# Performance work log

Measured on AMD Instinct MI355X. Metric: run time of the kernel, lower is better.

The kernel has to match this reference:

```python
import jax, jax.numpy as jnp
import numpy as np

B, C, W, H = 4, 256, 64, 64
N = W * H
SCALE = 0.02  # keep QK^T energies in a stable softmax range


def setup_inputs() -> dict:
    key = jax.random.key(0)
    ks = jax.random.split(key, 8)
    return {
        "x": jax.random.normal(ks[0], (B, C, W, H), jnp.float32),
        "geo_embed": jax.random.normal(ks[1], (B, N, C), jnp.float32),
        "Wq": jax.random.normal(ks[2], (C, C), jnp.float32) * SCALE,
        "bq": jnp.zeros((C,), jnp.float32),
        "Wk": jax.random.normal(ks[3], (C, C), jnp.float32) * SCALE,
        "bk": jnp.zeros((C,), jnp.float32),
        "Wv": jax.random.normal(ks[4], (C, C), jnp.float32) * SCALE,
        "bv": jnp.zeros((C,), jnp.float32),
        "Wgp": jax.random.normal(ks[5], (C, C), jnp.float32) * SCALE,
        "bgp": jnp.zeros((C,), jnp.float32),
        "Wgg": jax.random.normal(ks[6], (1, 2 * C), jnp.float32) * SCALE,
        "bgg": jnp.zeros((1,), jnp.float32),
    }


def reference(x, geo_embed, Wq, bq, Wk, bk, Wv, bv, Wgp, bgp, Wgg, bgg):
    b, c, w, h = x.shape
    n = w * h
    xf = x.reshape(b, c, n)  # [B, C, N]

    # 1x1 conv == per-pixel linear; q laid out [B, N, O] (permuted in torch)
    q = jnp.einsum("oc,bcn->bno", Wq, xf) + bq  # [B, N, O]

    # geo gating on the query
    ge = geo_embed @ Wgp.T + bgp  # [B, N, O]
    gate = jax.nn.sigmoid(jnp.concatenate([q, ge], axis=-1) @ Wgg.T + bgg)  # [B, N, 1]
    q = q + gate * ge

    k = jnp.einsum("oc,bcn->bon", Wk, xf) + bk[:, None]  # [B, O, N]
    v = jnp.einsum("oc,bcn->bon", Wv, xf) + bv[:, None]  # [B, C, N]

    energy = jnp.einsum("bno,bom->bnm", q, k)  # [B, N, N]
    attention = jax.nn.softmax(energy, axis=-1)

    # out = bmm(value, attention^T): out[b,c,m] = sum_n v[b,c,n] * attention[b,m,n]
    out = jnp.einsum("bcn,bmn->bcm", v, attention).reshape(b, c, w, h)

    # output gating: torch .view reinterpretation of (B, N, O) as (B, C, W, H)
    ge_r = ge.reshape(b, c, w, h)
    out = out * (1.0 + jax.nn.sigmoid(ge_r))
    return out, attention
```

## Files before the change

### kernel.cpp

```cpp
#include <hip/hip_runtime.h>
#include <hip/hip_bf16.h>
#include <math.h>

static constexpr int BB = 4;
static constexpr int CC = 256;
static constexpr int NN = 4096;

using bf16   = __bf16;
using f16    = _Float16;
using bf16x8 = __attribute__((ext_vector_type(8))) __bf16;
using bf16x4 = __attribute__((ext_vector_type(4))) __bf16;
using f16x8  = __attribute__((ext_vector_type(8))) _Float16;
using f16x4  = __attribute__((ext_vector_type(4))) _Float16;
using f32x4  = __attribute__((ext_vector_type(4))) float;

__device__ inline void gload_lds16(const void* g, void* l) {
  __builtin_amdgcn_global_load_lds(
      (const __attribute__((address_space(1))) void*)g,
      (__attribute__((address_space(3))) void*)l, 16, 0, 0);
}

__device__ inline void swz_bid(int& xb, int& yb, int& zb) {
  int gx = gridDim.x, gy = gridDim.y;
  int nwg = gx * gy * (int)gridDim.z;
  int flat = blockIdx.x + gx * (blockIdx.y + gy * blockIdx.z);
  int q = nwg >> 3;
  int w = (flat & 7) * q + (flat >> 3);
  xb = w % gx;
  int r = w / gx;
  yb = r % gy;
  zb = r / gy;
}

__global__ __launch_bounds__(256) void cvt_weights_kernel(
    const float* __restrict__ w0, const float* __restrict__ w1,
    const float* __restrict__ w2, const float* __restrict__ w3,
    bf16* __restrict__ out) {
  const float* srcs[4] = {w0, w1, w2, w3};
  const float* s = srcs[blockIdx.y];
  bf16* dst = out + (size_t)blockIdx.y * (CC * CC);
  int i = (blockIdx.x * 256 + threadIdx.x) * 4;
  float4 v = *(const float4*)(s + i);
  bf16x4 t;
  t[0] = (bf16)v.x; t[1] = (bf16)v.y; t[2] = (bf16)v.z; t[3] = (bf16)v.w;
  *(bf16x4*)(dst + i) = t;
}

__global__ __launch_bounds__(256) void cvt_f32_bf16_kernel(
    const float* __restrict__ in, bf16* __restrict__ out, long n) {
  long i = ((long)blockIdx.x * blockDim.x + threadIdx.x) * 4;
  if (i >= n) return;
  float4 v = *(const float4*)(in + i);
  bf16x4 t;
  t[0] = (bf16)v.x; t[1] = (bf16)v.y; t[2] = (bf16)v.z; t[3] = (bf16)v.w;
  *(bf16x4*)(out + i) = t;
}

__global__ __launch_bounds__(256) void transpose_x_kernel(
    const float* __restrict__ x, bf16* __restrict__ xt) {
  __shared__ float tile[64][65];
  int b  = blockIdx.z;
  int c0 = blockIdx.x * 64;
  int n0 = blockIdx.y * 64;
  const float* xp = x  + (long)b * CC * NN;
  bf16*       xtp = xt + (long)b * NN * CC;
  int tj = threadIdx.x & 63;
  int ti = threadIdx.x >> 6;
#pragma unroll
  for (int p = 0; p < 16; ++p) {
    int i = ti + p * 4;
    tile[i][tj] = xp[(long)(c0 + i) * NN + n0 + tj];
  }
  __syncthreads();
#pragma unroll
  for (int p = 0; p < 16; ++p) {
    int i = ti + p * 4;
    xtp[(long)(n0 + i) * CC + c0 + tj] = (bf16)tile[tj][i];
  }
}

__global__ __launch_bounds__(256) void proj_all_kernel(
    const bf16* __restrict__ xt, const bf16* __restrict__ geob,
    const bf16* __restrict__ Wall,
    const float* __restrict__ bq, const float* __restrict__ bgp,
    const float* __restrict__ bk, const float* __restrict__ bv,
    bf16* __restrict__ qn, float* __restrict__ ge,
    bf16* __restrict__ kn, bf16* __restrict__ vb) {
  __shared__ bf16 As[128 * 32];
  __shared__ bf16 Bs[128 * 32];
  const long NCst = (long)NN * CC;
  const int bz = blockIdx.z;
  const int b = bz >> 2, p = bz & 3;
  const bf16 *Ap, *Bp;
  const float* bias;
  int row0, col0;
  if (p == 3) {
    Ap = Wall + 2 * CC * CC;
    Bp = xt + b * NCst;
    bias = bv;
    row0 = blockIdx.x * 128;
    col0 = blockIdx.y * 128;
  } else {
    Ap = (p == 1 ? geob : xt) + b * NCst;
    Bp = Wall + (size_t)(p == 0 ? 0 : (p == 1 ? 3 : 1)) * CC * CC;
    bias = (p == 0 ? bq : (p == 1 ? bgp : bk));
    row0 = blockIdx.y * 128;
    col0 = blockIdx.x * 128;
  }

  const int t   = threadIdx.x;
  const int wid = t >> 6;
  const int l   = t & 63;
  const int lr  = l & 15;
  const int lk  = (l >> 4) * 8;
  const int warow = (wid >> 1) * 64;
  const int wbcol = (wid & 1) * 64;
  const int srow = t >> 2;
  const int scol = (t & 3) * 8;

  f32x4 acc[4][4];
#pragma unroll
  for (int i = 0; i < 4; ++i)
#pragma unroll
    for (int j = 0; j < 4; ++j) acc[i][j] = {0.f, 0.f, 0.f, 0.f};

  for (int k0 = 0; k0 < CC; k0 += 32) {
    __syncthreads();
#pragma unroll
    for (int q = 0; q < 2; ++q)
      gload_lds16(Ap + (long)(row0 + srow + 64 * q) * CC + k0 + scol,
                  As + ((q * 256 + t) * 8));
#pragma unroll
    for (int q = 0; q < 2; ++q)
      gload_lds16(Bp + (long)(col0 + srow + 64 * q) * CC + k0 + scol,
                  Bs + ((q * 256 + t) * 8));
    __syncthreads();
    bf16x8 a[4], bb[4];
#pragma unroll
    for (int i = 0; i < 4; ++i)
      a[i] = *(const bf16x8*)(As + (warow + 16 * i + lr) * 32 + lk);
#pragma unroll
    for (int j = 0; j < 4; ++j)
      bb[j] = *(const bf16x8*)(Bs + (wbcol + 16 * j + lr) * 32 + lk);
#pragma unroll
    for (int i = 0; i < 4; ++i)
#pragma unroll
      for (int j = 0; j < 4; ++j)
        acc[i][j] = __builtin_amdgcn_mfma_f32_16x16x32_bf16(a[i], bb[j], acc[i][j], 0, 0, 0);
  }

  const int orow = (l >> 4) * 4;
  const int ocol = l & 15;
#pragma unroll
  for (int i = 0; i < 4; ++i) {
#pragma unroll
    for (int j = 0; j < 4; ++j) {
      int colb = col0 + wbcol + 16 * j + ocol;
#pragma unroll
      for (int r = 0; r < 4; ++r) {
        int row = row0 + warow + 16 * i + orow + r;
        if (p == 3) {
          float vv = acc[i][j][r] + bias[row];
          vb[b * NCst + (long)row * NN + colb] = (bf16)vv;
        } else {
          float vv = acc[i][j][r] + bias[colb];
          long di = b * NCst + (long)row * CC + colb;
          if (p == 1)
            ge[di] = vv;
          else
            (p == 0 ? qn : kn)[di] = (bf16)vv;
        }
      }
    }
  }
}

template <int BIAS_MODE, int B_MODE, int OUT_MODE, bool GATE_EPI, bool SWZ, bool STAT>
__global__ __launch_bounds__(256) void gemm_nt_lds(
    const bf16* __restrict__ A, const void* __restrict__ Bm,
    const float* __restrict__ bias, void* __restrict__ D,
    const float* __restrict__ gefl, float2* __restrict__ pstat,
    int Ncols, int K, long sA, long sB, long sD, long sGe) {
  __shared__ bf16 As[128 * 32];
  __shared__ bf16 Bs[128 * 32];
  int bx = blockIdx.x, by = blockIdx.y, bz = blockIdx.z;
  if constexpr (SWZ) swz_bid(bx, by, bz);
  const bf16* Ab = A + (long)bz * sA;
  const float* geb = GATE_EPI ? (gefl + bz * sGe) : nullptr;

  const int t   = threadIdx.x;
  const int wid = t >> 6;
  const int l   = t & 63;
  const int lr  = l & 15;
  const int lk  = (l >> 4) * 8;
  const int row0 = by * 128;
  const int col0 = bx * 128;
  const int warow = (wid >> 1) * 64;
  const int wbcol = (wid & 1) * 64;

  const int srow = t >> 2;
  const int scol = (t & 3) * 8;
  const int frow = t >> 3;
  const int fc4  = (t & 7) * 4;

  f32x4 acc[4][4];
#pragma unroll
  for (int i = 0; i < 4; ++i)
#pragma unroll
    for (int j = 0; j < 4; ++j) acc[i][j] = {0.f, 0.f, 0.f, 0.f};

  for (int k0 = 0; k0 < K; k0 += 32) {
    __syncthreads();
#pragma unroll
    for (int p = 0; p < 2; ++p)
      gload_lds16(Ab + (long)(row0 + srow + 64 * p) * K + k0 + scol,
                  As + ((p * 256 + t) * 8));
    if constexpr (B_MODE == 0) {
      const bf16* Bb = (const bf16*)Bm + (long)bz * sB;
#pragma unroll
      for (int p = 0; p < 2; ++p)
        gload_lds16(Bb + (long)(col0 + srow + 64 * p) * K + k0 + scol,
                    Bs + ((p * 256 + t) * 8));
    } else {
      const float* Bf = (const float*)Bm + (long)bz * sB;
#pragma unroll
      for (int p = 0; p < 4; ++p) {
        float4 u = *(const float4*)(Bf + (long)(col0 + frow + 32 * p) * K + k0 + fc4);
        bf16x4 tv;
        tv[0] = (bf16)u.x; tv[1] = (bf16)u.y; tv[2] = (bf16)u.z; tv[3] = (bf16)u.w;
        *(bf16x4*)(Bs + (frow + 32 * p) * 32 + fc4) = tv;
      }
    }
    __syncthreads();
    bf16x8 a[4], bb[4];
#pragma unroll
    for (int i = 0; i < 4; ++i)
      a[i] = *(const bf16x8*)(As + (warow + 16 * i + lr) * 32 + lk);
#pragma unroll
    for (int j = 0; j < 4; ++j)
      bb[j] = *(const bf16x8*)(Bs + (wbcol + 16 * j + lr) * 32 + lk);
#pragma unroll
    for (int i = 0; i < 4; ++i)
#pragma unroll
      for (int j = 0; j < 4; ++j)
        acc[i][j] = __builtin_amdgcn_mfma_f32_16x16x32_bf16(a[i], bb[j], acc[i][j], 0, 0, 0);
  }

  const int orow = (l >> 4) * 4;
  const int ocol = l & 15;
#pragma unroll
  for (int i = 0; i < 4; ++i) {
#pragma unroll
    for (int j = 0; j < 4; ++j) {
      int colb = col0 + wbcol + 16 * j + ocol;
#pragma unroll
      for (int r = 0; r < 4; ++r) {
        int row = row0 + warow + 16 * i + orow + r;
        float vv = acc[i][j][r];
        if constexpr (BIAS_MODE == 1) vv += bias[colb];
        if constexpr (BIAS_MODE == 2) vv += bias[row];
        if constexpr (GATE_EPI) {
          float g = geb[(long)row * 4096 + colb];
          vv *= 1.f + 1.f / (1.f + __expf(-g));
        }
        long di = bz * sD + (long)row * Ncols + colb;
        if constexpr (OUT_MODE == 0)
          ((float*)D)[di] = vv;
        else if constexpr (OUT_MODE == 1)
          ((bf16*)D)[di] = (bf16)vv;
        else
          ((f16*)D)[di] = (f16)vv;
      }
    }
  }

  if constexpr (STAT) {
    __shared__ float2 sm[128][2];
#pragma unroll
    for (int i = 0; i < 4; ++i) {
#pragma unroll
      for (int r = 0; r < 4; ++r) {
        float m = fmaxf(fmaxf(acc[i][0][r], acc[i][1][r]),
                        fmaxf(acc[i][2][r], acc[i][3][r]));
#pragma unroll
        for (int s = 8; s >= 1; s >>= 1) m = fmaxf(m, __shfl_xor(m, s, 64));
        float sum = 0.f;
#pragma unroll
        for (int j = 0; j < 4; ++j) sum += __expf(acc[i][j][r] - m);
#pragma unroll
        for (int s = 8; s >= 1; s >>= 1) sum += __shfl_xor(sum, s, 64);
        if ((l & 15) == 0) {
          int Rl = warow + 16 * i + (l >> 4) * 4 + r;
          sm[Rl][wid & 1] = make_float2(m, sum);
        }
      }
    }
    __syncthreads();
    if (t < 128) {
      float2 a2 = sm[t][0], b2 = sm[t][1];
      float m = fmaxf(a2.x, b2.x);
      float s = a2.y * __expf(a2.x - m) + b2.y * __expf(b2.x - m);
      pstat[((long)bz * NN + row0 + t) * 32 + bx] = make_float2(m, s);
    }
  }
}

__global__ __launch_bounds__(256) void rowstat_reduce_kernel(
    const float2* __restrict__ pstat, float2* __restrict__ minv) {
  int row = blockIdx.x * 4 + (threadIdx.x >> 6);
  int l = threadIdx.x & 63;
  float2 v = (l < 32) ? pstat[(long)row * 32 + l] : make_float2(-1e30f, 0.f);
  float m = v.x;
#pragma unroll
  for (int s = 16; s >= 1; s >>= 1) m = fmaxf(m, __shfl_xor(m, s, 64));
  float sum = v.y * __expf(v.x - m);
#pragma unroll
  for (int s = 16; s >= 1; s >>= 1) sum += __shfl_xor(sum, s, 64);
  if (l == 0) minv[row] = make_float2(m, 1.f / sum);
}

template <bool SWZ>
__global__ __launch_bounds__(512) void pv_fused_kernel(
    const bf16* __restrict__ V, const f16* __restrict__ E,
    const float2* __restrict__ minv, float* __restrict__ attn,
    float* __restrict__ pbuf) {
  __shared__ bf16 Bs[2][64 * 64];
  int bx = blockIdx.x, by = blockIdx.y, bz = blockIdx.z;
  if constexpr (SWZ) swz_bid(bx, by, bz);
  const int mrow0 = bx * 64;
  const int KBASE = by * (NN / 2);
  const long NCst = (long)NN * CC;
  const long NNst = (long)NN * NN;
  const bf16* Vb = V + bz * NCst;
  const f16*  Eb = E + bz * NNst;
  float* attnb = attn + bz * NNst;
  float* pb = pbuf + (long)(bz * 2 + by) * NCst;

  const int t   = threadIdx.x;
  const int wid = t >> 6;
  const int l   = t & 63;
  const int lr  = l & 15;
  const int lk8 = l >> 4;
  const int crow = wid * 32;

  const int rE = t >> 3;
  const int q4 = (t & 7) * 4;
  const float2 mi = minv[(long)bz * NN + mrow0 + rE];
  const f16* Erow = Eb + (long)(mrow0 + rE) * NN + q4;
  float* Arow = attnb + (long)(mrow0 + rE) * NN + q4;
  const int c8a = (t & 7) >> 1;
  const int o4  = (t & 1) * 4;
  const int woff1 = rE * 64 + ((c8a ^ (rE & 7)) << 3) + o4;
  const int woff2 = rE * 64 + (((c8a + 4) ^ (rE & 7)) << 3) + o4;

  const bf16* Vr0 = Vb + (long)(crow + lr) * NN + lk8 * 8;
  const bf16* Vr1 = Vb + (long)(crow + 16 + lr) * NN + lk8 * 8;

  f32x4 acc[2][4];
#pragma unroll
  for (int i = 0; i < 2; ++i)
#pragma unroll
    for (int j = 0; j < 4; ++j) acc[i][j] = {0.f, 0.f, 0.f, 0.f};

  f16x4 elo = *(const f16x4*)(Erow + KBASE);
  f16x4 ehi = *(const f16x4*)(Erow + KBASE + 32);

  auto produce = [&](int kdst, int buf) {
    float pl[4], ph[4];
#pragma unroll
    for (int i = 0; i < 4; ++i) pl[i] = __expf((float)elo[i] - mi.x) * mi.y;
#pragma unroll
    for (int i = 0; i < 4; ++i) ph[i] = __expf((float)ehi[i] - mi.x) * mi.y;
    float4 u0 = {pl[0], pl[1], pl[2], pl[3]};
    float4 u1 = {ph[0], ph[1], ph[2], ph[3]};
    *(float4*)(Arow + kdst)      = u0;
    *(float4*)(Arow + kdst + 32) = u1;
    bf16x4 b0, b1;
#pragma unroll
    for (int i = 0; i < 4; ++i) { b0[i] = (bf16)pl[i]; b1[i] = (bf16)ph[i]; }
    *(bf16x4*)(&Bs[buf][woff1]) = b0;
    *(bf16x4*)(&Bs[buf][woff2]) = b1;
    int kn = (kdst + 64) & (NN - 1);
    elo = *(const f16x4*)(Erow + kn);
    ehi = *(const f16x4*)(Erow + kn + 32);
  };

  auto consume = [&](int buf, bf16x8 a00, bf16x8 a01, bf16x8 a10, bf16x8 a11) {
    const bf16* B0 = &Bs[buf][0];
#pragma unroll
    for (int j = 0; j < 4; ++j) {
      int Rb = 16 * j + lr;
      bf16x8 b0 = *(const bf16x8*)(B0 + Rb * 64 + ((lk8 ^ (Rb & 7)) * 8));
      bf16x8 b1 = *(const bf16x8*)(B0 + Rb * 64 + (((lk8 + 4) ^ (Rb & 7)) * 8));
      acc[0][j] = __builtin_amdgcn_mfma_f32_16x16x32_bf16(a00, b0, acc[0][j], 0, 0, 0);
      acc[1][j] = __builtin_amdgcn_mfma_f32_16x16x32_bf16(a10, b0, acc[1][j], 0, 0, 0);
      acc[0][j] = __builtin_amdgcn_mfma_f32_16x16x32_bf16(a01, b1, acc[0][j], 0, 0, 0);
      acc[1][j] = __builtin_amdgcn_mfma_f32_16x16x32_bf16(a11, b1, acc[1][j], 0, 0, 0);
    }
  };

#define LOADV(k0, A0, A1, A2, A3)                  \
  A0 = *(const bf16x8*)(Vr0 + (k0));               \
  A1 = *(const bf16x8*)(Vr0 + (k0) + 32);          \
  A2 = *(const bf16x8*)(Vr1 + (k0));               \
  A3 = *(const bf16x8*)(Vr1 + (k0) + 32);

#define FENCE_BAR()                                         \
  asm volatile("s_waitcnt lgkmcnt(0)" ::: "memory");        \
  __builtin_amdgcn_s_barrier();                             \
  __builtin_amdgcn_sched_barrier(0);

  bf16x8 A00, A01, A10, A11, B00, B01, B10, B11;

  produce(KBASE, 0);
  LOADV(KBASE, A00, A01, A10, A11);
  FENCE_BAR();

  for (int it = 0; it < 15; ++it) {
    int k0 = KBASE + it * 128;
    LOADV(k0 + 64, B00, B01, B10, B11);
    consume(0, A00, A01, A10, A11);
    produce(k0 + 64, 1);
    FENCE_BAR();
    LOADV(k0 + 128, A00, A01, A10, A11);
    consume(1, B00, B01, B10, B11);
    produce(k0 + 128, 0);
    FENCE_BAR();
  }
  LOADV(KBASE + 1984, B00, B01, B10, B11);
  consume(0, A00, A01, A10, A11);
  produce(KBASE + 1984, 1);
  FENCE_BAR();
  consume(1, B00, B01, B10, B11);
#undef LOADV
#undef FENCE_BAR

  const int orow = (l >> 4) * 4;
  const int ocol = l & 15;
#pragma unroll
  for (int i = 0; i < 2; ++i) {
#pragma unroll
    for (int j = 0; j < 4; ++j) {
      int m = mrow0 + 16 * j + ocol;
#pragma unroll
      for (int r = 0; r < 4; ++r) {
        int c = crow + 16 * i + orow + r;
        pb[(long)c * 4096 + m] = acc[i][j][r];
      }
    }
  }
}

__global__ __launch_bounds__(256) void combine_kernel(
    const float* __restrict__ pbuf, const float* __restrict__ ge,
    float* __restrict__ out) {
  const long NCst = (long)NN * CC;
  long i = ((long)blockIdx.x * 256 + threadIdx.x) * 8;
  int b = (int)(i >> 20);
  long r = i & (NCst - 1);
  const float* p0 = pbuf + (long)(b * 2) * NCst + r;
  const float* p1 = p0 + NCst;
  const float* g  = ge + (long)b * NCst + r;
  float* o = out + i;
#pragma unroll
  for (int h = 0; h < 2; ++h) {
    float4 a = *(const float4*)(p0 + h * 4);
    float4 c = *(const float4*)(p1 + h * 4);
    float4 gv = *(const float4*)(g + h * 4);
    float4 u;
    u.x = (a.x + c.x) * (1.f + 1.f / (1.f + __expf(-gv.x)));
    u.y = (a.y + c.y) * (1.f + 1.f / (1.f + __expf(-gv.y)));
    u.z = (a.z + c.z) * (1.f + 1.f / (1.f + __expf(-gv.z)));
    u.w = (a.w + c.w) * (1.f + 1.f / (1.f + __expf(-gv.w)));
    *(float4*)(o + h * 4) = u;
  }
}

__global__ __launch_bounds__(256) void gate_kernel(
    bf16* __restrict__ q, const float* __restrict__ ge,
    const float* __restrict__ Wgg, const float* __restrict__ bgg) {
  int row = blockIdx.x * 4 + (threadIdx.x >> 6);
  int l = threadIdx.x & 63;
  bf16* qr = q + (long)row * 256;
  const float* ger = ge + (long)row * 256;
  float s = 0.f;
  float qv[4], gv[4];
#pragma unroll
  for (int i = 0; i < 4; ++i) {
    int o = l + 64 * i;
    qv[i] = (float)qr[o];
    gv[i] = ger[o];
    s += qv[i] * Wgg[o] + gv[i] * Wgg[256 + o];
  }
#pragma unroll
  for (int m = 32; m >= 1; m >>= 1) s += __shfl_xor(s, m, 64);
  float gate = 1.f / (1.f + __expf(-(s + bgg[0])));
#pragma unroll
  for (int i = 0; i < 4; ++i) {
    int o = l + 64 * i;
    qr[o] = (bf16)(qv[i] + gate * gv[i]);
  }
}

__global__ __launch_bounds__(256) void softmax32_kernel(float* __restrict__ attn) {
  long row = blockIdx.x;
  float* p = attn + row * 4096;
  int t = threadIdx.x;
  __shared__ float red[8];
  float4 v[4];
  float mx = -1e30f;
#pragma unroll
  for (int c = 0; c < 4; ++c) {
    v[c] = *(const float4*)(p + c * 1024 + t * 4);
    mx = fmaxf(mx, fmaxf(fmaxf(v[c].x, v[c].y), fmaxf(v[c].z, v[c].w)));
  }
#pragma unroll
  for (int m = 32; m >= 1; m >>= 1) mx = fmaxf(mx, __shfl_xor(mx, m, 64));
  if ((t & 63) == 0) red[t >> 6] = mx;
  __syncthreads();
  mx = fmaxf(fmaxf(red[0], red[1]), fmaxf(red[2], red[3]));
  float sum = 0.f;
#pragma unroll
  for (int c = 0; c < 4; ++c) {
    v[c].x = __expf(v[c].x - mx);
    v[c].y = __expf(v[c].y - mx);
    v[c].z = __expf(v[c].z - mx);
    v[c].w = __expf(v[c].w - mx);
    sum += v[c].x + v[c].y + v[c].z + v[c].w;
  }
#pragma unroll
  for (int m = 32; m >= 1; m >>= 1) sum += __shfl_xor(sum, m, 64);
  if ((t & 63) == 0) red[4 + (t >> 6)] = sum;
  __syncthreads();
  float inv = 1.f / (red[4] + red[5] + red[6] + red[7]);
#pragma unroll
  for (int c = 0; c < 4; ++c) {
    v[c].x *= inv; v[c].y *= inv; v[c].z *= inv; v[c].w *= inv;
    *(float4*)(p + c * 1024 + t * 4) = v[c];
  }
}

extern "C" void kernel_launch(void* const* d_in, const int* in_sizes, int n_in,
                              void* d_out, int out_size, void* d_ws, size_t ws_size,
                              hipStream_t stream) {
  const float* x    = (const float*)d_in[0];
  const float* geo  = (const float*)d_in[1];
  const float* Wq   = (const float*)d_in[2];
  const float* bq   = (const float*)d_in[3];
  const float* Wk   = (const float*)d_in[4];
  const float* bk   = (const float*)d_in[5];
  const float* Wv   = (const float*)d_in[6];
  const float* bv   = (const float*)d_in[7];
  const float* Wgp  = (const float*)d_in[8];
  const float* bgp  = (const float*)d_in[9];
  const float* Wgg  = (const float*)d_in[10];
  const float* bgg  = (const float*)d_in[11];

  float* out  = (float*)d_out;
  float* attn = out + (long)BB * CC * NN;

  char* w = (char*)d_ws;
  size_t used = 0;
  auto alloc = [&](size_t bytes) {
    char* p = w + used;
    used += (bytes + 255) & ~(size_t)255;
    return p;
  };
  bf16*  xt   = (bf16*)alloc((size_t)BB * NN * CC * 2);
  bf16*  geob = (bf16*)alloc((size_t)BB * NN * CC * 2);
  bf16*  qn   = (bf16*)alloc((size_t)BB * NN * CC * 2);
  bf16*  kn   = (bf16*)alloc((size_t)BB * NN * CC * 2);
  bf16*  vb   = (bf16*)alloc((size_t)BB * CC * NN * 2);
  float* ge   = (float*)alloc((size_t)BB * NN * CC * 4);
  bf16*  Wall = (bf16*)alloc((size_t)4 * CC * CC * 2);
  bf16*  Wvb  = Wall + 2 * CC * CC;
  size_t abf_bytes   = (size_t)BB * NN * NN * 2;
  size_t pstat_bytes = (size_t)BB * NN * 32 * sizeof(float2);
  size_t minv_bytes  = (size_t)BB * NN * sizeof(float2);
  size_t pbuf_bytes  = (size_t)BB * 2 * NN * CC * 4;
  bool big = (ws_size >=
              used + abf_bytes + pstat_bytes + minv_bytes + pbuf_bytes + 2048);
  f16* abf = nullptr;
  float2* pstat = nullptr;
  float2* minv = nullptr;
  float* pbuf = nullptr;
  if (big) {
    abf   = (f16*)alloc(abf_bytes);
    pstat = (float2*)alloc(pstat_bytes);
    minv  = (float2*)alloc(minv_bytes);
    pbuf  = (float*)alloc(pbuf_bytes);
  }

  const long NCst = (long)NN * CC;
  const long NNst = (long)NN * NN;

  cvt_weights_kernel<<<dim3(64, 4), 256, 0, stream>>>(Wq, Wk, Wv, Wgp, Wall);
  cvt_f32_bf16_kernel<<<(BB * NCst) / 1024, 256, 0, stream>>>(geo, geob, BB * NCst);
  transpose_x_kernel<<<dim3(4, 64, BB), 256, 0, stream>>>(x, xt);

  proj_all_kernel<<<dim3(2, 32, BB * 4), 256, 0, stream>>>(
      xt, geob, Wall, bq, bgp, bk, bv, qn, ge, kn, vb);
  gate_kernel<<<(BB * NN) / 4, 256, 0, stream>>>(qn, ge, Wgg, bgg);

  if (big) {
    gemm_nt_lds<0, 0, 2, false, true, true><<<dim3(32, 32, BB), 256, 0, stream>>>(
        qn, kn, nullptr, abf, nullptr, pstat, NN, CC, NCst, NCst, NNst, 0);
    rowstat_reduce_kernel<<<(BB * NN) / 4, 256, 0, stream>>>(pstat, minv);
    pv_fused_kernel<true><<<dim3(64, 2, BB), 512, 0, stream>>>(
        vb, abf, minv, attn, pbuf);
    combine_kernel<<<(int)((long)BB * NCst / (256 * 8)), 256, 0, stream>>>(
        pbuf, ge, out);
  } else {
    gemm_nt_lds<0, 0, 0, false, true, false><<<dim3(32, 32, BB), 256, 0, stream>>>(
        qn, kn, nullptr, attn, nullptr, nullptr, NN, CC, NCst, NCst, NNst, 0);
    softmax32_kernel<<<BB * NN, 256, 0, stream>>>(attn);
    gemm_nt_lds<0, 1, 0, true, true, false><<<dim3(32, 2, BB), 256, 0, stream>>>(
        vb, attn, nullptr, out, ge, nullptr, NN, NN, NCst, NNst, NCst, NCst);
  }
}
```

Measured before the change: 300.3 us.

## Fuse geo conversion into projection, store ge as fp16, add dedicated energy kernel

Removes the separate geo_embed fp32-to-bf16 conversion kernel by converting inside the projection GEMM's A-tile load, and stores the projected ge in fp16 instead of fp32, halving its traffic in the gate, combine and fallback kernels. Adds a dedicated 512-thread energy kernel with 256x128 tiles, a 64-wide k-step and XOR-swizzled LDS that writes fp16 energies and per-tile softmax stats. Switches the large attention and partial-output stores to nontemporal stores. The fp16 ge adds rounding error, and the inline conversion path for geo uses plain loads instead of async LDS loads.

```diff
diff --git a/kernel.cpp b/kernel.cpp
--- a/kernel.cpp
+++ b/kernel.cpp
@@ -46,16 +46,6 @@
   *(bf16x4*)(dst + i) = t;
 }
 
-__global__ __launch_bounds__(256) void cvt_f32_bf16_kernel(
-    const float* __restrict__ in, bf16* __restrict__ out, long n) {
-  long i = ((long)blockIdx.x * blockDim.x + threadIdx.x) * 4;
-  if (i >= n) return;
-  float4 v = *(const float4*)(in + i);
-  bf16x4 t;
-  t[0] = (bf16)v.x; t[1] = (bf16)v.y; t[2] = (bf16)v.z; t[3] = (bf16)v.w;
-  *(bf16x4*)(out + i) = t;
-}
-
 __global__ __launch_bounds__(256) void transpose_x_kernel(
     const float* __restrict__ x, bf16* __restrict__ xt) {
   __shared__ float tile[64][65];
@@ -80,18 +70,19 @@
 }
 
 __global__ __launch_bounds__(256) void proj_all_kernel(
-    const bf16* __restrict__ xt, const bf16* __restrict__ geob,
+    const bf16* __restrict__ xt, const float* __restrict__ geo,
     const bf16* __restrict__ Wall,
     const float* __restrict__ bq, const float* __restrict__ bgp,
     const float* __restrict__ bk, const float* __restrict__ bv,
-    bf16* __restrict__ qn, float* __restrict__ ge,
+    bf16* __restrict__ qn, f16* __restrict__ ge,
     bf16* __restrict__ kn, bf16* __restrict__ vb) {
   __shared__ bf16 As[128 * 32];
   __shared__ bf16 Bs[128 * 32];
   const long NCst = (long)NN * CC;
   const int bz = blockIdx.z;
   const int b = bz >> 2, p = bz & 3;
-  const bf16 *Ap, *Bp;
+  const bf16 *Ap = nullptr, *Bp;
+  const float* Af32 = nullptr;
   const float* bias;
   int row0, col0;
   if (p == 3) {
@@ -101,7 +92,8 @@
     row0 = blockIdx.x * 128;
     col0 = blockIdx.y * 128;
   } else {
-    Ap = (p == 1 ? geob : xt) + b * NCst;
+    if (p == 1) Af32 = geo + b * NCst;
+    else        Ap   = xt + b * NCst;
     Bp = Wall + (size_t)(p == 0 ? 0 : (p == 1 ? 3 : 1)) * CC * CC;
     bias = (p == 0 ? bq : (p == 1 ? bgp : bk));
     row0 = blockIdx.y * 128;
@@ -117,6 +109,8 @@
   const int wbcol = (wid & 1) * 64;
   const int srow = t >> 2;
   const int scol = (t & 3) * 8;
+  const int frow = t >> 3;
+  const int fc4  = (t & 7) * 4;
 
   f32x4 acc[4][4];
 #pragma unroll
@@ -126,10 +120,20 @@
 
   for (int k0 = 0; k0 < CC; k0 += 32) {
     __syncthreads();
-#pragma unroll
-    for (int q = 0; q < 2; ++q)
-      gload_lds16(Ap + (long)(row0 + srow + 64 * q) * CC + k0 + scol,
-                  As + ((q * 256 + t) * 8));
+    if (p == 1) {
+#pragma unroll
+      for (int q = 0; q < 4; ++q) {
+        float4 u = *(const float4*)(Af32 + (long)(row0 + frow + 32 * q) * CC + k0 + fc4);
+        bf16x4 tv;
+        tv[0] = (bf16)u.x; tv[1] = (bf16)u.y; tv[2] = (bf16)u.z; tv[3] = (bf16)u.w;
+        *(bf16x4*)(As + (frow + 32 * q) * 32 + fc4) = tv;
+      }
+    } else {
+#pragma unroll
+      for (int q = 0; q < 2; ++q)
+        gload_lds16(Ap + (long)(row0 + srow + 64 * q) * CC + k0 + scol,
+                    As + ((q * 256 + t) * 8));
+    }
 #pragma unroll
     for (int q = 0; q < 2; ++q)
       gload_lds16(Bp + (long)(col0 + srow + 64 * q) * CC + k0 + scol,
@@ -166,7 +170,7 @@
           float vv = acc[i][j][r] + bias[colb];
           long di = b * NCst + (long)row * CC + colb;
           if (p == 1)
-            ge[di] = vv;
+            ge[di] = (f16)vv;
           else
             (p == 0 ? qn : kn)[di] = (bf16)vv;
         }
@@ -175,18 +179,131 @@
   }
 }
 
-template <int BIAS_MODE, int B_MODE, int OUT_MODE, bool GATE_EPI, bool SWZ, bool STAT>
+template <bool SWZ>
+__global__ __launch_bounds__(512) void energy_kernel(
+    const bf16* __restrict__ Q, const bf16* __restrict__ K,
+    f16* __restrict__ E, float2* __restrict__ pstat) {
+  __shared__ bf16 As[256 * 64];
+  __shared__ bf16 Bs[128 * 64];
+  __shared__ float2 sm[256][2];
+  int bx = blockIdx.x, by = blockIdx.y, bz = blockIdx.z;
+  if constexpr (SWZ) swz_bid(bx, by, bz);
+  const long NCst = (long)NN * CC;
+  const long NNst = (long)NN * NN;
+  const bf16* Qb = Q + bz * NCst;
+  const bf16* Kb = K + bz * NCst;
+  f16* Eb = E + bz * NNst;
+  const int row0 = by * 256;
+  const int col0 = bx * 128;
+
+  const int t   = threadIdx.x;
+  const int wid = t >> 6;
+  const int l   = t & 63;
+  const int lr  = l & 15;
+  const int lk8 = l >> 4;
+  const int wm  = (wid >> 1) * 64;
+  const int wn  = (wid & 1) * 64;
+
+  const int srow = t >> 3;
+  const int schk = t & 7;
+
+  f32x4 acc[4][4];
+#pragma unroll
+  for (int i = 0; i < 4; ++i)
+#pragma unroll
+    for (int j = 0; j < 4; ++j) acc[i][j] = {0.f, 0.f, 0.f, 0.f};
+
+  for (int k0 = 0; k0 < CC; k0 += 64) {
+    __syncthreads();
+#pragma unroll
+    for (int p = 0; p < 4; ++p) {
+      int r = srow + 64 * p;
+      gload_lds16(Qb + (long)(row0 + r) * CC + k0 + ((schk ^ (r & 7)) * 8),
+                  As + ((p * 512 + t) * 8));
+    }
+#pragma unroll
+    for (int p = 0; p < 2; ++p) {
+      int r = srow + 64 * p;
+      gload_lds16(Kb + (long)(col0 + r) * CC + k0 + ((schk ^ (r & 7)) * 8),
+                  Bs + ((p * 512 + t) * 8));
+    }
+    __syncthreads();
+#pragma unroll
+    for (int kk = 0; kk < 2; ++kk) {
+      bf16x8 a[4], b[4];
+#pragma unroll
+      for (int i = 0; i < 4; ++i) {
+        int Ra = wm + 16 * i + lr;
+        a[i] = *(const bf16x8*)(As + Ra * 64 + (((kk * 4 + lk8) ^ (Ra & 7)) * 8));
+      }
+#pragma unroll
+      for (int j = 0; j < 4; ++j) {
+        int Rb = wn + 16 * j + lr;
+        b[j] = *(const bf16x8*)(Bs + Rb * 64 + (((kk * 4 + lk8) ^ (Rb & 7)) * 8));
+      }
+#pragma unroll
+      for (int i = 0; i < 4; ++i)
+#pragma unroll
+        for (int j = 0; j < 4; ++j)
+          acc[i][j] = __builtin_amdgcn_mfma_f32_16x16x32_bf16(a[i], b[j], acc[i][j], 0, 0, 0);
+    }
+  }
+
+  const int orow = (l >> 4) * 4;
+  const int ocol = l & 15;
+#pragma unroll
+  for (int i = 0; i < 4; ++i) {
+#pragma unroll
+    for (int j = 0; j < 4; ++j) {
+      int colb = col0 + wn + 16 * j + ocol;
+#pragma unroll
+      for (int r = 0; r < 4; ++r) {
+        int row = row0 + wm + 16 * i + orow + r;
+        Eb[(long)row * NN + colb] = (f16)acc[i][j][r];
+      }
+    }
+  }
+
+#pragma unroll
+  for (int i = 0; i < 4; ++i) {
+#pragma unroll
+    for (int r = 0; r < 4; ++r) {
+      float m = fmaxf(fmaxf(acc[i][0][r], acc[i][1][r]),
+                      fmaxf(acc[i][2][r], acc[i][3][r]));
+#pragma unroll
+      for (int s = 8; s >= 1; s >>= 1) m = fmaxf(m, __shfl_xor(m, s, 64));
+      float sum = 0.f;
+#pragma unroll
+      for (int j = 0; j < 4; ++j) sum += __expf(acc[i][j][r] - m);
+#pragma unroll
+      for (int s = 8; s >= 1; s >>= 1) sum += __shfl_xor(sum, s, 64);
+      if ((l & 15) == 0) {
+        int Rl = wm + 16 * i + (l >> 4) * 4 + r;
+        sm[Rl][wid & 1] = make_float2(m, sum);
+      }
+    }
+  }
+  __syncthreads();
+  if (t < 256) {
+    float2 a2 = sm[t][0], b2 = sm[t][1];
+    float m = fmaxf(a2.x, b2.x);
+    float s = a2.y * __expf(a2.x - m) + b2.y * __expf(b2.x - m);
+    pstat[((long)bz * NN + row0 + t) * 32 + bx] = make_float2(m, s);
+  }
+}
+
+template <int BIAS_MODE, int B_MODE, int OUT_MODE, bool GATE_EPI, bool SWZ>
 __global__ __launch_bounds__(256) void gemm_nt_lds(
     const bf16* __restrict__ A, const void* __restrict__ Bm,
     const float* __restrict__ bias, void* __restrict__ D,
-    const float* __restrict__ gefl, float2* __restrict__ pstat,
+    const f16* __restrict__ gefl,
     int Ncols, int K, long sA, long sB, long sD, long sGe) {
   __shared__ bf16 As[128 * 32];
   __shared__ bf16 Bs[128 * 32];
   int bx = blockIdx.x, by = blockIdx.y, bz = blockIdx.z;
   if constexpr (SWZ) swz_bid(bx, by, bz);
   const bf16* Ab = A + (long)bz * sA;
-  const float* geb = GATE_EPI ? (gefl + bz * sGe) : nullptr;
+  const f16* geb = GATE_EPI ? (gefl + bz * sGe) : nullptr;
 
   const int t   = threadIdx.x;
   const int wid = t >> 6;
@@ -260,7 +377,7 @@
         if constexpr (BIAS_MODE == 1) vv += bias[colb];
         if constexpr (BIAS_MODE == 2) vv += bias[row];
         if constexpr (GATE_EPI) {
-          float g = geb[(long)row * 4096 + colb];
+          float g = (float)geb[(long)row * 4096 + colb];
           vv *= 1.f + 1.f / (1.f + __expf(-g));
         }
         long di = bz * sD + (long)row * Ncols + colb;
@@ -271,36 +388,6 @@
         else
           ((f16*)D)[di] = (f16)vv;
       }
-    }
-  }
-
-  if constexpr (STAT) {
-    __shared__ float2 sm[128][2];
-#pragma unroll
-    for (int i = 0; i < 4; ++i) {
-#pragma unroll
-      for (int r = 0; r < 4; ++r) {
-        float m = fmaxf(fmaxf(acc[i][0][r], acc[i][1][r]),
-                        fmaxf(acc[i][2][r], acc[i][3][r]));
-#pragma unroll
-        for (int s = 8; s >= 1; s >>= 1) m = fmaxf(m, __shfl_xor(m, s, 64));
-        float sum = 0.f;
-#pragma unroll
-        for (int j = 0; j < 4; ++j) sum += __expf(acc[i][j][r] - m);
-#pragma unroll
-        for (int s = 8; s >= 1; s >>= 1) sum += __shfl_xor(sum, s, 64);
-        if ((l & 15) == 0) {
-          int Rl = warow + 16 * i + (l >> 4) * 4 + r;
-          sm[Rl][wid & 1] = make_float2(m, sum);
-        }
-      }
-    }
-    __syncthreads();
-    if (t < 128) {
-      float2 a2 = sm[t][0], b2 = sm[t][1];
-      float m = fmaxf(a2.x, b2.x);
-      float s = a2.y * __expf(a2.x - m) + b2.y * __expf(b2.x - m);
-      pstat[((long)bz * NN + row0 + t) * 32 + bx] = make_float2(m, s);
     }
   }
 }
@@ -371,10 +458,10 @@
     for (int i = 0; i < 4; ++i) pl[i] = __expf((float)elo[i] - mi.x) * mi.y;
 #pragma unroll
     for (int i = 0; i < 4; ++i) ph[i] = __expf((float)ehi[i] - mi.x) * mi.y;
-    float4 u0 = {pl[0], pl[1], pl[2], pl[3]};
-    float4 u1 = {ph[0], ph[1], ph[2], ph[3]};
-    *(float4*)(Arow + kdst)      = u0;
-    *(float4*)(Arow + kdst + 32) = u1;
+    f32x4 u0 = {pl[0], pl[1], pl[2], pl[3]};
+    f32x4 u1 = {ph[0], ph[1], ph[2], ph[3]};
+    __builtin_nontemporal_store(u0, (f32x4*)(Arow + kdst));
+    __builtin_nontemporal_store(u1, (f32x4*)(Arow + kdst + 32));
     bf16x4 b0, b1;
 #pragma unroll
     for (int i = 0; i < 4; ++i) { b0[i] = (bf16)pl[i]; b1[i] = (bf16)ph[i]; }
@@ -445,14 +532,14 @@
 #pragma unroll
       for (int r = 0; r < 4; ++r) {
         int c = crow + 16 * i + orow + r;
-        pb[(long)c * 4096 + m] = acc[i][j][r];
+        __builtin_nontemporal_store(acc[i][j][r], pb + (long)c * 4096 + m);
       }
     }
   }
 }
 
 __global__ __launch_bounds__(256) void combine_kernel(
-    const float* __restrict__ pbuf, const float* __restrict__ ge,
+    const float* __restrict__ pbuf, const f16* __restrict__ ge,
     float* __restrict__ out) {
   const long NCst = (long)NN * CC;
   long i = ((long)blockIdx.x * 256 + threadIdx.x) * 8;
@@ -460,36 +547,36 @@
   long r = i & (NCst - 1);
   const float* p0 = pbuf + (long)(b * 2) * NCst + r;
   const float* p1 = p0 + NCst;
-  const float* g  = ge + (long)b * NCst + r;
+  const f16* g = ge + (long)b * NCst + r;
   float* o = out + i;
+  f16x8 gv = *(const f16x8*)(g);
 #pragma unroll
   for (int h = 0; h < 2; ++h) {
     float4 a = *(const float4*)(p0 + h * 4);
     float4 c = *(const float4*)(p1 + h * 4);
-    float4 gv = *(const float4*)(g + h * 4);
     float4 u;
-    u.x = (a.x + c.x) * (1.f + 1.f / (1.f + __expf(-gv.x)));
-    u.y = (a.y + c.y) * (1.f + 1.f / (1.f + __expf(-gv.y)));
-    u.z = (a.z + c.z) * (1.f + 1.f / (1.f + __expf(-gv.z)));
-    u.w = (a.w + c.w) * (1.f + 1.f / (1.f + __expf(-gv.w)));
+    u.x = (a.x + c.x) * (1.f + 1.f / (1.f + __expf(-(float)gv[4 * h + 0])));
+    u.y = (a.y + c.y) * (1.f + 1.f / (1.f + __expf(-(float)gv[4 * h + 1])));
+    u.z = (a.z + c.z) * (1.f + 1.f / (1.f + __expf(-(float)gv[4 * h + 2])));
+    u.w = (a.w + c.w) * (1.f + 1.f / (1.f + __expf(-(float)gv[4 * h + 3])));
     *(float4*)(o + h * 4) = u;
   }
 }
 
 __global__ __launch_bounds__(256) void gate_kernel(
-    bf16* __restrict__ q, const float* __restrict__ ge,
+    bf16* __restrict__ q, const f16* __restrict__ ge,
     const float* __restrict__ Wgg, const float* __restrict__ bgg) {
   int row = blockIdx.x * 4 + (threadIdx.x >> 6);
   int l = threadIdx.x & 63;
   bf16* qr = q + (long)row * 256;
-  const float* ger = ge + (long)row * 256;
+  const f16* ger = ge + (long)row * 256;
   float s = 0.f;
   float qv[4], gv[4];
 #pragma unroll
   for (int i = 0; i < 4; ++i) {
     int o = l + 64 * i;
     qv[i] = (float)qr[o];
-    gv[i] = ger[o];
+    gv[i] = (float)ger[o];
     s += qv[i] * Wgg[o] + gv[i] * Wgg[256 + o];
   }
 #pragma unroll
@@ -567,13 +654,11 @@
     return p;
   };
   bf16*  xt   = (bf16*)alloc((size_t)BB * NN * CC * 2);
-  bf16*  geob = (bf16*)alloc((size_t)BB * NN * CC * 2);
   bf16*  qn   = (bf16*)alloc((size_t)BB * NN * CC * 2);
   bf16*  kn   = (bf16*)alloc((size_t)BB * NN * CC * 2);
   bf16*  vb   = (bf16*)alloc((size_t)BB * CC * NN * 2);
-  float* ge   = (float*)alloc((size_t)BB * NN * CC * 4);
+  f16*   ge   = (f16*)alloc((size_t)BB * NN * CC * 2);
   bf16*  Wall = (bf16*)alloc((size_t)4 * CC * CC * 2);
-  bf16*  Wvb  = Wall + 2 * CC * CC;
   size_t abf_bytes   = (size_t)BB * NN * NN * 2;
   size_t pstat_bytes = (size_t)BB * NN * 32 * sizeof(float2);
   size_t minv_bytes  = (size_t)BB * NN * sizeof(float2);
@@ -595,26 +680,25 @@
   const long NNst = (long)NN * NN;
 
   cvt_weights_kernel<<<dim3(64, 4), 256, 0, stream>>>(Wq, Wk, Wv, Wgp, Wall);
-  cvt_f32_bf16_kernel<<<(BB * NCst) / 1024, 256, 0, stream>>>(geo, geob, BB * NCst);
   transpose_x_kernel<<<dim3(4, 64, BB), 256, 0, stream>>>(x, xt);
 
   proj_all_kernel<<<dim3(2, 32, BB * 4), 256, 0, stream>>>(
-      xt, geob, Wall, bq, bgp, bk, bv, qn, ge, kn, vb);
+      xt, geo, Wall, bq, bgp, bk, bv, qn, ge, kn, vb);
   gate_kernel<<<(BB * NN) / 4, 256, 0, stream>>>(qn, ge, Wgg, bgg);
 
   if (big) {
-    gemm_nt_lds<0, 0, 2, false, true, true><<<dim3(32, 32, BB), 256, 0, stream>>>(
-        qn, kn, nullptr, abf, nullptr, pstat, NN, CC, NCst, NCst, NNst, 0);
+    energy_kernel<true><<<dim3(32, 16, BB), 512, 0, stream>>>(
+        qn, kn, abf, pstat);
     rowstat_reduce_kernel<<<(BB * NN) / 4, 256, 0, stream>>>(pstat, minv);
     pv_fused_kernel<true><<<dim3(64, 2, BB), 512, 0, stream>>>(
         vb, abf, minv, attn, pbuf);
     combine_kernel<<<(int)((long)BB * NCst / (256 * 8)), 256, 0, stream>>>(
         pbuf, ge, out);
   } else {
-    gemm_nt_lds<0, 0, 0, false, true, false><<<dim3(32, 32, BB), 256, 0, stream>>>(
-        qn, kn, nullptr, attn, nullptr, nullptr, NN, CC, NCst, NCst, NNst, 0);
+    gemm_nt_lds<0, 0, 0, false, true><<<dim3(32, 32, BB), 256, 0, stream>>>(
+        qn, kn, nullptr, attn, nullptr, NN, CC, NCst, NCst, NNst, 0);
     softmax32_kernel<<<BB * NN, 256, 0, stream>>>(attn);
-    gemm_nt_lds<0, 1, 0, true, true, false><<<dim3(32, 2, BB), 256, 0, stream>>>(
-        vb, attn, nullptr, out, ge, nullptr, NN, NN, NCst, NNst, NCst, NCst);
-  }
-}
+    gemm_nt_lds<0, 1, 0, true, true><<<dim3(32, 2, BB), 256, 0, stream>>>(
+        vb, attn, nullptr, out, ge, NN, NN, NCst, NNst, NCst, NCst);
+  }
+}
```

After: 256.5 us. 14.6% less time.
